# Kernel optimization log

Measured on AMD Instinct MI355X. Metric: run time of the kernel, lower is better.

## Reference

```python
import jax, jax.numpy as jnp
import numpy as np

# Transformer-XL relative multi-head attention (eval mode, dropout = identity)
B, Q, M, D, H = 2, 1024, 1024, 1024, 16
DH = D // H          # 64 head dim
K = Q + M            # key length = memory + current segment
SCALE = 0.02         # param init scale


def setup_inputs() -> dict:
    key = jax.random.key(0)
    ks = jax.random.split(key, 10)
    return {
        "inputs": jax.random.normal(ks[0], (B, Q, D), jnp.float32),
        "inputs_mem": jax.random.normal(ks[1], (B, M, D), jnp.float32),
        "r": jax.random.normal(ks[2], (B, K, D), jnp.float32),
        "W_qkv": jax.random.normal(ks[3], (D, 3 * D), jnp.float32) * SCALE,
        "b_qkv": jnp.zeros((3 * D,), jnp.float32),
        "W_r": jax.random.normal(ks[4], (D, D), jnp.float32) * SCALE,
        "b_r": jnp.zeros((D,), jnp.float32),
        "W_o": jax.random.normal(ks[5], (D, D), jnp.float32) * SCALE,
        "b_o": jnp.zeros((D,), jnp.float32),
        "u": jax.random.normal(ks[6], (1, H, 1, DH), jnp.float32) * SCALE,
        "v": jax.random.normal(ks[7], (1, H, 1, DH), jnp.float32) * SCALE,
    }


def _split_heads(x):
    # [B, L, D] -> [B, H, L, DH]
    b, l, _ = x.shape
    return x.reshape(b, l, H, DH).transpose(0, 2, 1, 3)


def _rel_shift(x):
    # Transformer-XL relative shift: pad one zero column on the left,
    # reshape to [B, H, K+1, Q], drop first row, reshape back.
    b, h, q, k = x.shape
    x = jnp.pad(x, ((0, 0), (0, 0), (0, 0), (1, 0)))
    x = x.reshape(b, h, k + 1, q)[:, :, 1:, :]
    return x.reshape(b, h, q, k)


def reference(inputs, inputs_mem, r, W_qkv, b_qkv, W_r, b_r, W_o, b_o, u, v):
    cat = jnp.concatenate([inputs_mem, inputs], axis=1)      # [B, K, D]
    w = cat @ W_qkv + b_qkv                                   # [B, K, 3D]
    rp = r @ W_r + b_r                                        # [B, K, D]
    # NOTE: source splits as (q, v, k) in that order
    w_q, w_v, w_k = jnp.split(w, 3, axis=-1)
    hq = _split_heads(w_q)[:, :, -Q:]                          # [B, H, Q, DH]
    hk = _split_heads(w_k)                                     # [B, H, K, DH]
    hv = _split_heads(w_v)                                     # [B, H, K, DH]
    hr = _split_heads(rp)                                      # [B, H, K, DH]
    ac = jnp.einsum('bhqd,bhkd->bhqk', hq + u, hk)             # content term
    bd = _rel_shift(jnp.einsum('bhqd,bhkd->bhqk', hq + v, hr)) # position term
    score = (ac + bd) / (DH ** 0.5)
    # causal mask with memory: query i attends to all mem + positions <= i
    mem_len = K - Q
    mask = (jnp.arange(K)[None, :] <= mem_len + jnp.arange(Q)[:, None]).astype(jnp.float32)
    score = score * mask - 1e30 * (1.0 - mask)
    weights = jax.nn.softmax(score, axis=-1)                   # [B, H, Q, K]
    out = jnp.einsum('bhqk,bhkd->bhqd', weights, hv)           # [B, H, Q, DH]
    out = out.transpose(0, 2, 1, 3).reshape(B, Q, D)
    return out @ W_o + b_o
```

## Files before the change

kernel.cpp:

```cpp
#include <hip/hip_runtime.h>
#include <hip/hip_bf16.h>
#include <stdint.h>


typedef __bf16 bf16;
typedef __bf16 bf16x2 __attribute__((ext_vector_type(2)));
typedef __bf16 bf16x4 __attribute__((ext_vector_type(4)));
typedef __bf16 bf16x8 __attribute__((ext_vector_type(8)));
typedef float  f32x4  __attribute__((ext_vector_type(4)));

__device__ __forceinline__ void async_copy16(void* lds, const void* g) {
    auto gp = (const __attribute__((address_space(1))) void*)(uintptr_t)g;
    auto lp = (__attribute__((address_space(3))) void*)(uint32_t)(uintptr_t)lds;
    __builtin_amdgcn_global_load_lds(gp, lp, 16, 0, 0);
}

__device__ __forceinline__ void gemm128_core(
    const bf16* __restrict__ A, const bf16* __restrict__ Bt, const int Kd,
    const int m0, const int n0, bf16* As, bf16* Bs, f32x4 acc[4][4])
{
    const int tid  = threadIdx.x;
    const int lane = tid & 63;
    const int wave = tid >> 6;
    const int wr   = (wave >> 1) * 64;
    const int wc   = (wave & 1) * 64;
    const int lr   = lane & 15;
    const int q4   = lane >> 4;

#pragma unroll
    for (int i = 0; i < 4; ++i)
#pragma unroll
        for (int j = 0; j < 4; ++j) {
            acc[i][j][0] = 0.f; acc[i][j][1] = 0.f; acc[i][j][2] = 0.f; acc[i][j][3] = 0.f;
        }

    auto stage = [&](int buf, int k0) {
#pragma unroll
        for (int it = 0; it < 2; ++it) {
            const int cb0   = (it * 4 + wave) * 64;
            const int chunk = cb0 + lane;
            const int row   = chunk >> 2;
            const int cg    = (chunk & 3) * 8;
            async_copy16(As + buf * 4096 + cb0 * 8, A  + (size_t)(m0 + row) * Kd + k0 + cg);
            async_copy16(Bs + buf * 4096 + cb0 * 8, Bt + (size_t)(n0 + row) * Kd + k0 + cg);
        }
    };

    const int NT = Kd >> 5;
    stage(0, 0);
    __syncthreads();

    for (int t = 0; t < NT; ++t) {
        const int buf = t & 1;
        if (t + 1 < NT) stage(buf ^ 1, (t + 1) * 32);

        const bf16* Ab = As + buf * 4096;
        const bf16* Bb = Bs + buf * 4096;
        bf16x8 af[4], bfr[4];
#pragma unroll
        for (int rb = 0; rb < 4; ++rb)
            af[rb] = *(const bf16x8*)&Ab[(wr + rb * 16 + lr) * 32 + q4 * 8];
#pragma unroll
        for (int cb = 0; cb < 4; ++cb)
            bfr[cb] = *(const bf16x8*)&Bb[(wc + cb * 16 + lr) * 32 + q4 * 8];
#pragma unroll
        for (int rb = 0; rb < 4; ++rb)
#pragma unroll
            for (int cb = 0; cb < 4; ++cb)
                acc[rb][cb] = __builtin_amdgcn_mfma_f32_16x16x32_bf16(af[rb], bfr[cb], acc[rb][cb], 0, 0, 0);
        __syncthreads();
    }
}

__device__ __forceinline__ void gemm64_core(
    const bf16* __restrict__ A, const bf16* __restrict__ Bt, const int Kd,
    const int m0, const int n0, bf16* As, bf16* Bs, f32x4 acc[2][4])
{
    const int tid  = threadIdx.x;
    const int lane = tid & 63;
    const int wave = tid >> 6;
    const int wr   = (wave >> 1) * 32;
    const int wc   = (wave & 1) * 64;
    const int lr   = lane & 15;
    const int q4   = lane >> 4;

#pragma unroll
    for (int i = 0; i < 2; ++i)
#pragma unroll
        for (int j = 0; j < 4; ++j) {
            acc[i][j][0] = 0.f; acc[i][j][1] = 0.f; acc[i][j][2] = 0.f; acc[i][j][3] = 0.f;
        }

    auto stage = [&](int buf, int k0) {
        {
            const int chunk = tid;
            const int row   = chunk >> 2;
            const int cg    = (chunk & 3) * 8;
            async_copy16(As + buf * 2048 + (wave * 64) * 8, A + (size_t)(m0 + row) * Kd + k0 + cg);
        }
#pragma unroll
        for (int it = 0; it < 2; ++it) {
            const int cb0   = (it * 4 + wave) * 64;
            const int chunk = cb0 + lane;
            const int row   = chunk >> 2;
            const int cg    = (chunk & 3) * 8;
            async_copy16(Bs + buf * 4096 + cb0 * 8, Bt + (size_t)(n0 + row) * Kd + k0 + cg);
        }
    };

    const int NT = Kd >> 5;
    stage(0, 0);
    __syncthreads();

    for (int t = 0; t < NT; ++t) {
        const int buf = t & 1;
        if (t + 1 < NT) stage(buf ^ 1, (t + 1) * 32);

        const bf16* Ab = As + buf * 2048;
        const bf16* Bb = Bs + buf * 4096;
        bf16x8 af[2], bfr[4];
#pragma unroll
        for (int rb = 0; rb < 2; ++rb)
            af[rb] = *(const bf16x8*)&Ab[(wr + rb * 16 + lr) * 32 + q4 * 8];
#pragma unroll
        for (int cb = 0; cb < 4; ++cb)
            bfr[cb] = *(const bf16x8*)&Bb[(wc + cb * 16 + lr) * 32 + q4 * 8];
#pragma unroll
        for (int rb = 0; rb < 2; ++rb)
#pragma unroll
            for (int cb = 0; cb < 4; ++cb)
                acc[rb][cb] = __builtin_amdgcn_mfma_f32_16x16x32_bf16(af[rb], bfr[cb], acc[rb][cb], 0, 0, 0);
        __syncthreads();
    }
}

__global__ __launch_bounds__(256) void k_prep(
    const float* __restrict__ Wqkv, const float* __restrict__ Wr,
    const float* __restrict__ Wo,
    const float* __restrict__ mem, const float* __restrict__ inp,
    const float* __restrict__ r,
    bf16* __restrict__ Wqkvt, bf16* __restrict__ Wrt, bf16* __restrict__ Wot,
    bf16* __restrict__ catb, bf16* __restrict__ rb)
{
    __shared__ float t[32][33];
    int id = blockIdx.x;
    if (id < 5120) {
        const float* in; bf16* out; int C, bx, by;
        if (id < 3072)      { in = Wqkv; out = Wqkvt; C = 3072; bx = id % 96; by = id / 96; }
        else if (id < 4096) { id -= 3072; in = Wr; out = Wrt; C = 1024; bx = id & 31; by = id >> 5; }
        else                { id -= 4096; in = Wo; out = Wot; C = 1024; bx = id & 31; by = id >> 5; }
        const int R = 1024;
        const int c0 = bx * 32, r0 = by * 32;
        const int lc = threadIdx.x & 31, lrow = threadIdx.x >> 5;
#pragma unroll
        for (int p = 0; p < 4; ++p)
            t[lrow + p * 8][lc] = in[(size_t)(r0 + lrow + p * 8) * C + c0 + lc];
        __syncthreads();
#pragma unroll
        for (int p = 0; p < 4; ++p)
            out[(size_t)(c0 + lrow + p * 8) * R + r0 + lc] = (bf16)t[lc][lrow + p * 8];
    } else if (id < 9216) {
        const int e   = ((id - 5120) * 256 + threadIdx.x) * 4;
        const int row = e >> 10, dc = e & 1023;
        const int b   = row >> 11, k = row & 2047;
        const float* src = (k < 1024) ? mem + ((size_t)b * 1024 + k) * 1024 + dc
                                      : inp + ((size_t)b * 1024 + (k - 1024)) * 1024 + dc;
        float4 f = *(const float4*)src;
        bf16x4 o; o[0] = (bf16)f.x; o[1] = (bf16)f.y; o[2] = (bf16)f.z; o[3] = (bf16)f.w;
        *(bf16x4*)&catb[e] = o;
    } else {
        const int e = ((id - 9216) * 256 + threadIdx.x) * 4;
        float4 f = *(const float4*)(r + e);
        bf16x4 o; o[0] = (bf16)f.x; o[1] = (bf16)f.y; o[2] = (bf16)f.z; o[3] = (bf16)f.w;
        *(bf16x4*)&rb[e] = o;
    }
}

__global__ __launch_bounds__(256) void k_gemm_qkvr(
    const bf16* __restrict__ catb, const bf16* __restrict__ Wqkvt,
    const float* __restrict__ b_qkv, const float* __restrict__ u, const float* __restrict__ v,
    const bf16* __restrict__ rb_, const bf16* __restrict__ Wrt,
    const float* __restrict__ b_r,
    bf16* __restrict__ hq_u, bf16* __restrict__ hq_v,
    bf16* __restrict__ hk, bf16* __restrict__ hvT, bf16* __restrict__ hr)
{
    __shared__ bf16 lds[4 * 128 * 32];
    f32x4 acc[4][4];
    const int lane = threadIdx.x & 63, wave = threadIdx.x >> 6;
    const int wr = (wave >> 1) * 64, wc = (wave & 1) * 64;
    const int lr = lane & 15, q4 = lane >> 4;
    const int y = blockIdx.y;

    if (y < 16) {
        const int m0 = blockIdx.x * 128;
        const int n0 = 1024 + y * 128;
        gemm128_core(catb, Wqkvt, 1024, m0, n0, lds, lds + 2 * 4096, acc);
#pragma unroll
        for (int rb = 0; rb < 4; ++rb) {
#pragma unroll
            for (int cb = 0; cb < 4; ++cb) {
                const int col  = n0 + wc + cb * 16 + lr;
                const int part = col >> 10;
                const int hd   = col & 1023;
                const int h    = hd >> 6, d = hd & 63;
                const float bcol = b_qkv[col];
#pragma unroll
                for (int r = 0; r < 4; ++r) {
                    const int row = m0 + wr + rb * 16 + q4 * 4 + r;
                    const int b   = row >> 11, k = row & 2047;
                    const float val = acc[rb][cb][r] + bcol;
                    if (part == 1) {
                        hvT[(((size_t)(b * 16 + h)) * 64 + d) * 2048 + k] = (bf16)val;
                    } else {
                        hk[(((size_t)(b * 16 + h)) * 2048 + k) * 64 + d] = (bf16)val;
                    }
                }
            }
        }
    } else if (y < 20) {
        const int linear = (y - 16) * 32 + blockIdx.x;
        const int n0 = (linear & 7) * 128;
        const int mi = linear >> 3;
        const int m0 = (mi >> 3) * 2048 + 1024 + (mi & 7) * 128;
        gemm128_core(catb, Wqkvt, 1024, m0, n0, lds, lds + 2 * 4096, acc);
#pragma unroll
        for (int rb = 0; rb < 4; ++rb) {
#pragma unroll
            for (int cb = 0; cb < 4; ++cb) {
                const int col = n0 + wc + cb * 16 + lr;
                const int h = col >> 6, d = col & 63;
                const float bcol = b_qkv[col];
                const float uc = u[col], vc = v[col];
#pragma unroll
                for (int r = 0; r < 4; ++r) {
                    const int row = m0 + wr + rb * 16 + q4 * 4 + r;
                    const int b   = row >> 11, k = row & 2047;
                    const float val = acc[rb][cb][r] + bcol;
                    const size_t o = (((size_t)(b * 16 + h)) * 1024 + (k - 1024)) * 64 + d;
                    hq_u[o] = (bf16)(val + uc);
                    hq_v[o] = (bf16)(val + vc);
                }
            }
        }
    } else {
        const int m0 = blockIdx.x * 128;
        const int n0 = (y - 20) * 128;
        gemm128_core(rb_, Wrt, 1024, m0, n0, lds, lds + 2 * 4096, acc);
#pragma unroll
        for (int rb = 0; rb < 4; ++rb) {
#pragma unroll
            for (int cb = 0; cb < 4; ++cb) {
                const int col = n0 + wc + cb * 16 + lr;
                const int h = col >> 6, d = col & 63;
                const float bcol = b_r[col];
#pragma unroll
                for (int r = 0; r < 4; ++r) {
                    const int row = m0 + wr + rb * 16 + q4 * 4 + r;
                    const int b = row >> 11, k = row & 2047;
                    hr[(((size_t)(b * 16 + h)) * 2048 + k) * 64 + d] = (bf16)(acc[rb][cb][r] + bcol);
                }
            }
        }
    }
}

__global__ __launch_bounds__(256) void k_gemm_out(
    const bf16* __restrict__ attn, const bf16* __restrict__ Wt,
    const float* __restrict__ bias, float* __restrict__ out)
{
    __shared__ bf16 lds[2 * 2048 + 2 * 4096];
    f32x4 acc[2][4];
    const int m0 = blockIdx.x * 64, n0 = blockIdx.y * 128;
    gemm64_core(attn, Wt, 1024, m0, n0, lds, lds + 2 * 2048, acc);

    const int lane = threadIdx.x & 63, wave = threadIdx.x >> 6;
    const int wr = (wave >> 1) * 32, wc = (wave & 1) * 64;
    const int lr = lane & 15, q4 = lane >> 4;
#pragma unroll
    for (int rb = 0; rb < 2; ++rb) {
#pragma unroll
        for (int cb = 0; cb < 4; ++cb) {
            const int col = n0 + wc + cb * 16 + lr;
            const float bcol = bias[col];
#pragma unroll
            for (int r = 0; r < 4; ++r) {
                const int row = m0 + wr + rb * 16 + q4 * 4 + r;
                out[(size_t)row * 1024 + col] = acc[rb][cb][r] + bcol;
            }
        }
    }
}

__global__ __launch_bounds__(256) void k_attn(
    const bf16* __restrict__ hq_u, const bf16* __restrict__ hq_v,
    const bf16* __restrict__ hk, const bf16* __restrict__ hvT,
    const bf16* __restrict__ hr, bf16* __restrict__ attn)
{
    __shared__ bf16 Ks[2][64][72];
    __shared__ bf16 Vt[2][64][72];
    __shared__ bf16 Rs[192 * 72];
    __shared__ bf16 U[4][1600];

    const int bh = blockIdx.y;
    const int qt = (bh & 16) ? (15 - (int)blockIdx.x) : (int)blockIdx.x;
    const int q0 = qt * 64;
    const int tid = threadIdx.x, lane = tid & 63, wave = tid >> 6;
    const int lr = lane & 15, q4 = lane >> 4;
    bf16* Uw = &U[wave][0];

    const int nt  = 17 + qt;
    const int m0c = 15 - qt;
    const size_t kvbase = (size_t)bh * 2048 * 64;

    const int ci0  = tid,        r0_ = ci0 >> 3,  c0_ = (ci0 & 7) * 8;
    const int ci1  = 256 + tid,  r1_ = ci1 >> 3,  c1_ = (ci1 & 7) * 8;

    bf16x8 kv0, kv1, vv0, vv1, rv0, rv1;
    auto load_kv = [&](int t) {
        const int k0 = t * 64;
        kv0 = *(const bf16x8*)&hk [kvbase + (size_t)(k0 + r0_) * 64 + c0_];
        kv1 = *(const bf16x8*)&hk [kvbase + (size_t)(k0 + r1_) * 64 + c1_];
        vv0 = *(const bf16x8*)&hvT[kvbase + (size_t)r0_ * 2048 + k0 + c0_];
        vv1 = *(const bf16x8*)&hvT[kvbase + (size_t)r1_ * 2048 + k0 + c1_];
    };
    auto load_r = [&](int c) {
        if (c * 64 < 2048) {
            rv0 = *(const bf16x8*)&hr[kvbase + (size_t)(c * 64 + r0_) * 64 + c0_];
            rv1 = *(const bf16x8*)&hr[kvbase + (size_t)(c * 64 + r1_) * 64 + c1_];
        } else {
#pragma unroll
            for (int z = 0; z < 8; ++z) { rv0[z] = (bf16)0.f; rv1[z] = (bf16)0.f; }
        }
    };
    auto write_kv = [&](int buf) {
        *(bf16x8*)&Ks[buf][r0_][c0_] = kv0;
        *(bf16x8*)&Ks[buf][r1_][c1_] = kv1;
        *(bf16x8*)&Vt[buf][r0_][c0_] = vv0;
        *(bf16x8*)&Vt[buf][r1_][c1_] = vv1;
    };
    auto write_r = [&](int slot) {
        *(bf16x8*)&Rs[(slot * 64 + r0_) * 72 + c0_] = rv0;
        *(bf16x8*)&Rs[(slot * 64 + r1_) * 72 + c1_] = rv1;
    };

    const size_t qrow = ((size_t)bh * 1024 + q0 + wave * 16 + lr) * 64;
    const bf16x8 qu0 = *(const bf16x8*)&hq_u[qrow + q4 * 8];
    const bf16x8 qu1 = *(const bf16x8*)&hq_u[qrow + 32 + q4 * 8];
    const bf16x8 qv0 = *(const bf16x8*)&hq_v[qrow + q4 * 8];
    const bf16x8 qv1 = *(const bf16x8*)&hq_v[qrow + 32 + q4 * 8];

    f32x4 Oacc[4];
#pragma unroll
    for (int i = 0; i < 4; ++i) { Oacc[i][0] = 0.f; Oacc[i][1] = 0.f; Oacc[i][2] = 0.f; Oacc[i][3] = 0.f; }
    float lp[4] = {0.f, 0.f, 0.f, 0.f};

    load_kv(0);  write_kv(0);
    load_r(m0c);     write_r(m0c % 3);
    load_r(m0c + 1); write_r((m0c + 1) % 3);
    __syncthreads();

    for (int t = 0; t < nt; ++t) {
        const int k0  = t * 64;
        const int mt  = m0c + t;
        const int s0  = mt % 3;
        const int s1  = (s0 + 1 == 3) ? 0 : s0 + 1;
        const int s2  = (s1 + 1 == 3) ? 0 : s1 + 1;
        const int buf = t & 1;
        const bool more = (t + 1 < nt);
        if (more) { load_kv(t + 1); load_r(mt + 2); }

        __builtin_amdgcn_s_setprio(1);
        f32x4 S[4];
#pragma unroll
        for (int cb = 0; cb < 4; ++cb) {
            const bf16x8 kf0 = *(const bf16x8*)&Ks[buf][cb * 16 + lr][q4 * 8];
            const bf16x8 kf1 = *(const bf16x8*)&Ks[buf][cb * 16 + lr][32 + q4 * 8];
            f32x4 z; z[0] = 0.f; z[1] = 0.f; z[2] = 0.f; z[3] = 0.f;
            z = __builtin_amdgcn_mfma_f32_16x16x32_bf16(qu0, kf0, z, 0, 0, 0);
            S[cb] = __builtin_amdgcn_mfma_f32_16x16x32_bf16(qu1, kf1, z, 0, 0, 0);
        }
#pragma unroll
        for (int jbi = 0; jbi < 5; ++jbi) {
            const int jb   = jbi + 3 - wave;
            const int rrow = ((jb & 4) ? s1 : s0) * 64 + (jb & 3) * 16 + lr;
            const bf16x8 rf0 = *(const bf16x8*)&Rs[rrow * 72 + q4 * 8];
            const bf16x8 rf1 = *(const bf16x8*)&Rs[rrow * 72 + 32 + q4 * 8];
            f32x4 z; z[0] = 0.f; z[1] = 0.f; z[2] = 0.f; z[3] = 0.f;
            z = __builtin_amdgcn_mfma_f32_16x16x32_bf16(qv0, rf0, z, 0, 0, 0);
            z = __builtin_amdgcn_mfma_f32_16x16x32_bf16(qv1, rf1, z, 0, 0, 0);
            bf16x4 pk;
            pk[0] = (bf16)z[0]; pk[1] = (bf16)z[1]; pk[2] = (bf16)z[2]; pk[3] = (bf16)z[3];
            *(bf16x4*)&Uw[(jbi * 16 + lr) * 20 + q4 * 4] = pk;
        }

        float bdv[4][4];
#pragma unroll
        for (int cb = 0; cb < 4; ++cb)
#pragma unroll
            for (int r = 0; r < 4; ++r) {
                const int tq = q4 * 4 + r;
                bdv[cb][r] = (float)Uw[(cb * 16 + lr + 15 - tq) * 20 + tq];
            }

#pragma unroll
        for (int cb = 0; cb < 4; ++cb) {
            const int k = k0 + cb * 16 + lr;
#pragma unroll
            for (int r = 0; r < 4; ++r) {
                const int q = q0 + wave * 16 + q4 * 4 + r;
                const float s = (S[cb][r] + bdv[cb][r]) * 0.125f;
                const float p = (k <= 1024 + q) ? __expf(s) : 0.f;
                lp[r] += p;
                Uw[(q4 * 4 + r) * 76 + cb * 16 + lr] = (bf16)p;
            }
        }

        const bf16x8 pf0 = *(const bf16x8*)&Uw[lr * 76 + q4 * 8];
        const bf16x8 pf1 = *(const bf16x8*)&Uw[lr * 76 + 32 + q4 * 8];
#pragma unroll
        for (int db = 0; db < 4; ++db) {
            const bf16x8 vf0 = *(const bf16x8*)&Vt[buf][db * 16 + lr][q4 * 8];
            const bf16x8 vf1 = *(const bf16x8*)&Vt[buf][db * 16 + lr][32 + q4 * 8];
            Oacc[db] = __builtin_amdgcn_mfma_f32_16x16x32_bf16(pf0, vf0, Oacc[db], 0, 0, 0);
            Oacc[db] = __builtin_amdgcn_mfma_f32_16x16x32_bf16(pf1, vf1, Oacc[db], 0, 0, 0);
        }
        __builtin_amdgcn_s_setprio(0);

        if (more) {
            write_kv(buf ^ 1);
            write_r(s2);
            __syncthreads();
        }
    }

#pragma unroll
    for (int off = 1; off < 16; off <<= 1)
#pragma unroll
        for (int r = 0; r < 4; ++r) lp[r] += __shfl_xor(lp[r], off, 64);

    const int b = bh >> 4, h = bh & 15;
#pragma unroll
    for (int r = 0; r < 4; ++r) {
        const float rl = 1.f / lp[r];
        const int q = q0 + wave * 16 + q4 * 4 + r;
#pragma unroll
        for (int db = 0; db < 4; ++db) {
            const int d = db * 16 + lr;
            attn[(((size_t)b * 1024 + q) * 16 + h) * 64 + d] = (bf16)(Oacc[db][r] * rl);
        }
    }
}

extern "C" void kernel_launch(void* const* d_in, const int* in_sizes, int n_in,
                              void* d_out, int out_size, void* d_ws, size_t ws_size,
                              hipStream_t stream)
{
    const float* inputs = (const float*)d_in[0];
    const float* mem    = (const float*)d_in[1];
    const float* r      = (const float*)d_in[2];
    const float* W_qkv  = (const float*)d_in[3];
    const float* b_qkv  = (const float*)d_in[4];
    const float* W_r    = (const float*)d_in[5];
    const float* b_r    = (const float*)d_in[6];
    const float* W_o    = (const float*)d_in[7];
    const float* b_o    = (const float*)d_in[8];
    const float* u      = (const float*)d_in[9];
    const float* v      = (const float*)d_in[10];
    float* out = (float*)d_out;

    char* ws = (char*)d_ws;
    size_t off = 0;
    auto alloc = [&](size_t bytes) -> void* {
        void* p = ws + off;
        off += (bytes + 255) & ~(size_t)255;
        return p;
    };
    bf16* hq_u  = (bf16*)alloc(2ull * 16 * 1024 * 64 * 2);
    bf16* hq_v  = (bf16*)alloc(2ull * 16 * 1024 * 64 * 2);
    bf16* hk    = (bf16*)alloc(2ull * 16 * 2048 * 64 * 2);
    bf16* hvT   = (bf16*)alloc(2ull * 16 * 2048 * 64 * 2);
    bf16* hr    = (bf16*)alloc(2ull * 16 * 2048 * 64 * 2);
    bf16* attnb = (bf16*)alloc(2ull * 1024 * 1024 * 2);
    bf16* Wot   = (bf16*)alloc(1024ull * 1024 * 2);
    bf16* catb  = (bf16*)alloc(4096ull * 1024 * 2);
    bf16* rb    = (bf16*)alloc(4096ull * 1024 * 2);
    bf16* Wqkvt = (bf16*)alloc(3072ull * 1024 * 2);
    bf16* Wrt   = (bf16*)alloc(1024ull * 1024 * 2);

    k_prep<<<13312, 256, 0, stream>>>(W_qkv, W_r, W_o, mem, inputs, r,
                                      Wqkvt, Wrt, Wot, catb, rb);

    k_gemm_qkvr<<<dim3(32, 28), 256, 0, stream>>>(catb, Wqkvt, b_qkv, u, v,
                                                  rb, Wrt, b_r,
                                                  hq_u, hq_v, hk, hvT, hr);
    k_attn<<<dim3(16, 32), 256, 0, stream>>>(hq_u, hq_v, hk, hvT, hr, attnb);
    k_gemm_out<<<dim3(32, 8), 256, 0, stream>>>(attnb, Wot, b_o, out);
}
```

Baseline: 248.8 us.

## Stage attention K/V/R tiles with async global-to-LDS copies and XOR swizzle

The attention kernel now loads the K, V^T and R tiles with direct global_load_lds 16-byte async copies instead of going through registers and separate LDS stores. This is meant to free registers and remove the store instructions from the loop. Because these copies cannot pad rows, the projection GEMM now writes hk, hvT and hr in an XOR-swizzled column order, so the attention kernel can use unpadded LDS rows without bank conflicts. In exchange, out-of-range R chunks are no longer zero-filled and will hold stale LDS data. Correctness also depends on the barrier waiting for the async loads to finish.

```diff
diff --git a/kernel.cpp b/kernel.cpp
--- a/kernel.cpp
+++ b/kernel.cpp
@@ -210,9 +210,11 @@
                     const int b   = row >> 11, k = row & 2047;
                     const float val = acc[rb][cb][r] + bcol;
                     if (part == 1) {
-                        hvT[(((size_t)(b * 16 + h)) * 64 + d) * 2048 + k] = (bf16)val;
+                        const int ks = (k & ~63) | ((k & 63) ^ ((d & 7) << 3));
+                        hvT[(((size_t)(b * 16 + h)) * 64 + d) * 2048 + ks] = (bf16)val;
                     } else {
-                        hk[(((size_t)(b * 16 + h)) * 2048 + k) * 64 + d] = (bf16)val;
+                        const int ds = d ^ ((k & 7) << 3);
+                        hk[(((size_t)(b * 16 + h)) * 2048 + k) * 64 + ds] = (bf16)val;
                     }
                 }
             }
@@ -257,7 +259,8 @@
                 for (int r = 0; r < 4; ++r) {
                     const int row = m0 + wr + rb * 16 + q4 * 4 + r;
                     const int b = row >> 11, k = row & 2047;
-                    hr[(((size_t)(b * 16 + h)) * 2048 + k) * 64 + d] = (bf16)(acc[rb][cb][r] + bcol);
+                    const int ds = d ^ ((k & 7) << 3);
+                    hr[(((size_t)(b * 16 + h)) * 2048 + k) * 64 + ds] = (bf16)(acc[rb][cb][r] + bcol);
                 }
             }
         }
@@ -296,9 +299,9 @@
     const bf16* __restrict__ hk, const bf16* __restrict__ hvT,
     const bf16* __restrict__ hr, bf16* __restrict__ attn)
 {
-    __shared__ bf16 Ks[2][64][72];
-    __shared__ bf16 Vt[2][64][72];
-    __shared__ bf16 Rs[192 * 72];
+    __shared__ bf16 Ks[2][64][64];
+    __shared__ bf16 Vt[2][64][64];
+    __shared__ bf16 Rs[192][64];
     __shared__ bf16 U[4][1600];
 
     const int bh = blockIdx.y;
@@ -312,35 +315,21 @@
     const int m0c = 15 - qt;
     const size_t kvbase = (size_t)bh * 2048 * 64;
 
-    const int ci0  = tid,        r0_ = ci0 >> 3,  c0_ = (ci0 & 7) * 8;
-    const int ci1  = 256 + tid,  r1_ = ci1 >> 3,  c1_ = (ci1 & 7) * 8;
-
-    bf16x8 kv0, kv1, vv0, vv1, rv0, rv1;
-    auto load_kv = [&](int t) {
+    const int r0_ = tid >> 3, c0_ = (tid & 7) * 8;
+    const int r1_ = 32 + r0_, c1_ = c0_;
+
+    auto stage_kv = [&](int t, int buf) {
         const int k0 = t * 64;
-        kv0 = *(const bf16x8*)&hk [kvbase + (size_t)(k0 + r0_) * 64 + c0_];
-        kv1 = *(const bf16x8*)&hk [kvbase + (size_t)(k0 + r1_) * 64 + c1_];
-        vv0 = *(const bf16x8*)&hvT[kvbase + (size_t)r0_ * 2048 + k0 + c0_];
-        vv1 = *(const bf16x8*)&hvT[kvbase + (size_t)r1_ * 2048 + k0 + c1_];
+        async_copy16(&Ks[buf][r0_][c0_], &hk [kvbase + (size_t)(k0 + r0_) * 64 + c0_]);
+        async_copy16(&Ks[buf][r1_][c1_], &hk [kvbase + (size_t)(k0 + r1_) * 64 + c1_]);
+        async_copy16(&Vt[buf][r0_][c0_], &hvT[kvbase + (size_t)r0_ * 2048 + k0 + c0_]);
+        async_copy16(&Vt[buf][r1_][c1_], &hvT[kvbase + (size_t)r1_ * 2048 + k0 + c1_]);
     };
-    auto load_r = [&](int c) {
+    auto stage_r = [&](int c, int slot) {
         if (c * 64 < 2048) {
-            rv0 = *(const bf16x8*)&hr[kvbase + (size_t)(c * 64 + r0_) * 64 + c0_];
-            rv1 = *(const bf16x8*)&hr[kvbase + (size_t)(c * 64 + r1_) * 64 + c1_];
-        } else {
-#pragma unroll
-            for (int z = 0; z < 8; ++z) { rv0[z] = (bf16)0.f; rv1[z] = (bf16)0.f; }
-        }
-    };
-    auto write_kv = [&](int buf) {
-        *(bf16x8*)&Ks[buf][r0_][c0_] = kv0;
-        *(bf16x8*)&Ks[buf][r1_][c1_] = kv1;
-        *(bf16x8*)&Vt[buf][r0_][c0_] = vv0;
-        *(bf16x8*)&Vt[buf][r1_][c1_] = vv1;
-    };
-    auto write_r = [&](int slot) {
-        *(bf16x8*)&Rs[(slot * 64 + r0_) * 72 + c0_] = rv0;
-        *(bf16x8*)&Rs[(slot * 64 + r1_) * 72 + c1_] = rv1;
+            async_copy16(&Rs[slot * 64 + r0_][c0_], &hr[kvbase + (size_t)(c * 64 + r0_) * 64 + c0_]);
+            async_copy16(&Rs[slot * 64 + r1_][c1_], &hr[kvbase + (size_t)(c * 64 + r1_) * 64 + c1_]);
+        }
     };
 
     const size_t qrow = ((size_t)bh * 1024 + q0 + wave * 16 + lr) * 64;
@@ -349,14 +338,18 @@
     const bf16x8 qv0 = *(const bf16x8*)&hq_v[qrow + q4 * 8];
     const bf16x8 qv1 = *(const bf16x8*)&hq_v[qrow + 32 + q4 * 8];
 
+    const int sw  = (lr & 7) << 3;
+    const int cA0 = (q4 * 8) ^ sw;
+    const int cA1 = (32 + q4 * 8) ^ sw;
+
     f32x4 Oacc[4];
 #pragma unroll
     for (int i = 0; i < 4; ++i) { Oacc[i][0] = 0.f; Oacc[i][1] = 0.f; Oacc[i][2] = 0.f; Oacc[i][3] = 0.f; }
     float lp[4] = {0.f, 0.f, 0.f, 0.f};
 
-    load_kv(0);  write_kv(0);
-    load_r(m0c);     write_r(m0c % 3);
-    load_r(m0c + 1); write_r((m0c + 1) % 3);
+    stage_kv(0, 0);
+    stage_r(m0c,     m0c % 3);
+    stage_r(m0c + 1, (m0c + 1) % 3);
     __syncthreads();
 
     for (int t = 0; t < nt; ++t) {
@@ -367,14 +360,14 @@
         const int s2  = (s1 + 1 == 3) ? 0 : s1 + 1;
         const int buf = t & 1;
         const bool more = (t + 1 < nt);
-        if (more) { load_kv(t + 1); load_r(mt + 2); }
+        if (more) { stage_kv(t + 1, buf ^ 1); stage_r(mt + 2, s2); }
 
         __builtin_amdgcn_s_setprio(1);
         f32x4 S[4];
 #pragma unroll
         for (int cb = 0; cb < 4; ++cb) {
-            const bf16x8 kf0 = *(const bf16x8*)&Ks[buf][cb * 16 + lr][q4 * 8];
-            const bf16x8 kf1 = *(const bf16x8*)&Ks[buf][cb * 16 + lr][32 + q4 * 8];
+            const bf16x8 kf0 = *(const bf16x8*)&Ks[buf][cb * 16 + lr][cA0];
+            const bf16x8 kf1 = *(const bf16x8*)&Ks[buf][cb * 16 + lr][cA1];
             f32x4 z; z[0] = 0.f; z[1] = 0.f; z[2] = 0.f; z[3] = 0.f;
             z = __builtin_amdgcn_mfma_f32_16x16x32_bf16(qu0, kf0, z, 0, 0, 0);
             S[cb] = __builtin_amdgcn_mfma_f32_16x16x32_bf16(qu1, kf1, z, 0, 0, 0);
@@ -383,8 +376,8 @@
         for (int jbi = 0; jbi < 5; ++jbi) {
             const int jb   = jbi + 3 - wave;
             const int rrow = ((jb & 4) ? s1 : s0) * 64 + (jb & 3) * 16 + lr;
-            const bf16x8 rf0 = *(const bf16x8*)&Rs[rrow * 72 + q4 * 8];
-            const bf16x8 rf1 = *(const bf16x8*)&Rs[rrow * 72 + 32 + q4 * 8];
+            const bf16x8 rf0 = *(const bf16x8*)&Rs[rrow][cA0];
+            const bf16x8 rf1 = *(const bf16x8*)&Rs[rrow][cA1];
             f32x4 z; z[0] = 0.f; z[1] = 0.f; z[2] = 0.f; z[3] = 0.f;
             z = __builtin_amdgcn_mfma_f32_16x16x32_bf16(qv0, rf0, z, 0, 0, 0);
             z = __builtin_amdgcn_mfma_f32_16x16x32_bf16(qv1, rf1, z, 0, 0, 0);
@@ -419,18 +412,14 @@
         const bf16x8 pf1 = *(const bf16x8*)&Uw[lr * 76 + 32 + q4 * 8];
 #pragma unroll
         for (int db = 0; db < 4; ++db) {
-            const bf16x8 vf0 = *(const bf16x8*)&Vt[buf][db * 16 + lr][q4 * 8];
-            const bf16x8 vf1 = *(const bf16x8*)&Vt[buf][db * 16 + lr][32 + q4 * 8];
+            const bf16x8 vf0 = *(const bf16x8*)&Vt[buf][db * 16 + lr][cA0];
+            const bf16x8 vf1 = *(const bf16x8*)&Vt[buf][db * 16 + lr][cA1];
             Oacc[db] = __builtin_amdgcn_mfma_f32_16x16x32_bf16(pf0, vf0, Oacc[db], 0, 0, 0);
             Oacc[db] = __builtin_amdgcn_mfma_f32_16x16x32_bf16(pf1, vf1, Oacc[db], 0, 0, 0);
         }
         __builtin_amdgcn_s_setprio(0);
 
-        if (more) {
-            write_kv(buf ^ 1);
-            write_r(s2);
-            __syncthreads();
-        }
+        if (more) __syncthreads();
     }
 
 #pragma unroll
```

Result: faster. 243.5 us (median of 2 runs) (-2.1%).
